# Performance work log

Measured on AMD Instinct MI355X. Metric: run time of the kernel, lower is better.

The kernel has to match this reference:

```python
import jax, jax.numpy as jnp
import numpy as np

B, S, E, H = 2, 2048, 1024, 16
D = E // H  # head_dim = 64
SCALE = D ** -0.5
NEG = -1e9


def setup_inputs() -> dict:
    key = jax.random.key(0)
    ks = jax.random.split(key, 10)
    hidden_states = jax.random.normal(ks[0], (B, S, E), dtype=jnp.float32)
    # CLIP-style additive causal mask [B, 1, L, S]
    causal = jnp.where(jnp.tril(jnp.ones((S, S), dtype=bool)), 0.0, NEG).astype(jnp.float32)
    attn_mask = jnp.broadcast_to(causal, (B, 1, S, S))
    def lin(kw, kb):
        W = jax.random.normal(kw, (E, E), dtype=jnp.float32) * (E ** -0.5)
        b = jax.random.normal(kb, (E,), dtype=jnp.float32) * 0.02
        return W, b
    Wq, bq = lin(ks[1], ks[2])
    Wk, bk = lin(ks[3], ks[4])
    Wv, bv = lin(ks[5], ks[6])
    Wo, bo = lin(ks[7], ks[8])
    return {"hidden_states": hidden_states, "attn_mask": attn_mask,
            "Wq": Wq, "bq": bq, "Wk": Wk, "bk": bk,
            "Wv": Wv, "bv": bv, "Wo": Wo, "bo": bo}


def reference(hidden_states, attn_mask, Wq, bq, Wk, bk, Wv, bv, Wo, bo):
    b, L, e = hidden_states.shape
    # projections (nn.Linear: x @ W.T + b)
    def split_heads(x):
        return x.reshape(b, L, H, D).transpose(0, 2, 1, 3)  # [b,h,l,d]
    q = split_heads(hidden_states @ Wq.T + bq)
    k = split_heads(hidden_states @ Wk.T + bk)
    v = split_heads(hidden_states @ Wv.T + bv)
    # QK^T * scale + additive mask, softmax, AV (dropout_p = 0 in eval)
    scores = jnp.einsum('bhld,bhsd->bhls', q, k) * SCALE + attn_mask
    attn = jax.nn.softmax(scores, axis=-1)
    ctx = jnp.einsum('bhls,bhsd->bhld', attn, v)
    ctx = ctx.transpose(0, 2, 1, 3).reshape(b, L, e)
    return ctx @ Wo.T + bo
```

## Files before the change

### kernel.cpp

```cpp
#include <hip/hip_runtime.h>
#include <hip/hip_bf16.h>
#include <stdint.h>


typedef __hip_bfloat16 bf16;
typedef short bf16x8 __attribute__((ext_vector_type(8)));
typedef short bf16x4 __attribute__((ext_vector_type(4)));
typedef float f32x4 __attribute__((ext_vector_type(4)));

__device__ __forceinline__ f32x4 mfma16(bf16x8 a, bf16x8 b, f32x4 c) {
  return __builtin_amdgcn_mfma_f32_16x16x32_bf16(a, b, c, 0, 0, 0);
}

__device__ __forceinline__ f32x4 mfma_k16(bf16x4 a, bf16x4 b, f32x4 c) {
#if __has_builtin(__builtin_amdgcn_mfma_f32_16x16x16bf16_1k)
  return __builtin_amdgcn_mfma_f32_16x16x16bf16_1k(a, b, c, 0, 0, 0);
#else
  f32x4 d;
  asm volatile("v_mfma_f32_16x16x16_bf16 %0, %1, %2, %3\n\ts_nop 7\n\ts_nop 7"
               : "=v"(d)
               : "v"(a), "v"(b), "v"(c));
  return d;
#endif
}

__device__ __forceinline__ void async16(const void* g, void* l) {
  __builtin_amdgcn_global_load_lds((const __attribute__((address_space(1))) void*)g,
                                   (__attribute__((address_space(3))) void*)l, 16, 0, 0);
}

__global__ __launch_bounds__(256) void cvt_kernel(
    const float* __restrict__ hs, const float* __restrict__ Wq,
    const float* __restrict__ Wk, const float* __restrict__ Wv,
    const float* __restrict__ Wo, bf16* __restrict__ dst) {
  const size_t e = ((size_t)blockIdx.x * 256 + threadIdx.x) * 8;
  const float* src;
  size_t off;
  if (e < 4194304) {
    src = hs; off = e;
  } else {
    const size_t w = e - 4194304;
    const int wi = (int)(w >> 20);
    src = (wi == 0) ? Wq : (wi == 1) ? Wk : (wi == 2) ? Wv : Wo;
    off = w & 1048575;
  }
  const float4 a = *(const float4*)(src + off);
  const float4 b = *(const float4*)(src + off + 4);
  union { bf16 h[8]; uint4 u; } p;
  p.h[0] = __float2bfloat16(a.x); p.h[1] = __float2bfloat16(a.y);
  p.h[2] = __float2bfloat16(a.z); p.h[3] = __float2bfloat16(a.w);
  p.h[4] = __float2bfloat16(b.x); p.h[5] = __float2bfloat16(b.y);
  p.h[6] = __float2bfloat16(b.z); p.h[7] = __float2bfloat16(b.w);
  *(uint4*)(dst + e) = p.u;
}

__global__ __launch_bounds__(256, 3) void qkv_gemm(
    const bf16* __restrict__ X, const bf16* __restrict__ Wb,
    const float* __restrict__ bq, const float* __restrict__ bk,
    const float* __restrict__ bv, bf16* __restrict__ out) {
  constexpr int Kd = 1024;
  __shared__ bf16 sA[2][128 * 32];
  __shared__ bf16 sB[2][128 * 32];
  const int tid = threadIdx.x;
  const int wave = tid >> 6, lane = tid & 63;
  const int g = lane >> 4, ln = lane & 15;
  const int tM = blockIdx.y * 128, tN = blockIdx.x * 128;
  const int which = tN >> 10;
  const bf16* W = Wb + (size_t)which * 1048576;
  const float* bias = (which == 0) ? bq : (which == 1) ? bk : bv;
  const int tNl = tN & 1023;
  const float oscale = (which == 0) ? 0.18033688011112042f : 1.0f;
  const int wrow = (wave >> 1) * 64, wcol = (wave & 1) * 64;
  const f32x4 fz = {0.f, 0.f, 0.f, 0.f};

  f32x4 acc[4][4];
#pragma unroll
  for (int i = 0; i < 4; ++i)
#pragma unroll
    for (int j = 0; j < 4; ++j) acc[i][j] = fz;

  int srow[4], scol[4];
#pragma unroll
  for (int t = 0; t < 4; ++t) {
    const int d = tid + t * 256;
    srow[t] = (d >> 2) & 127;
    scol[t] = ((d >> 9) << 5) + ((d & 3) << 3);
  }

  for (int k0 = 0; k0 < Kd; k0 += 64) {
    __syncthreads();
#pragma unroll
    for (int t = 0; t < 4; ++t) {
      const int d = tid + t * 256;
      async16(X + (size_t)(tM + srow[t]) * Kd + k0 + scol[t], &sA[0][0] + d * 8);
      async16(W + (size_t)(tNl + srow[t]) * Kd + k0 + scol[t], &sB[0][0] + d * 8);
    }
    __syncthreads();
#pragma unroll
    for (int kk = 0; kk < 2; ++kk) {
      bf16x8 aF[4], bF[4];
#pragma unroll
      for (int i = 0; i < 4; ++i)
        aF[i] = *(const bf16x8*)(&sA[kk][0] + (wrow + i * 16 + ln) * 32 + g * 8);
#pragma unroll
      for (int j = 0; j < 4; ++j)
        bF[j] = *(const bf16x8*)(&sB[kk][0] + (wcol + j * 16 + ln) * 32 + g * 8);
#pragma unroll
      for (int i = 0; i < 4; ++i)
#pragma unroll
        for (int j = 0; j < 4; ++j) acc[i][j] = mfma16(aF[i], bF[j], acc[i][j]);
    }
  }

  bf16* outw = out + (size_t)which * 4194304;
#pragma unroll
  for (int j = 0; j < 4; ++j) {
    const int nl = tNl + wcol + j * 16 + ln;
    const float bvf = bias[nl];
    const int h = nl >> 6, d = nl & 63;
#pragma unroll
    for (int i = 0; i < 4; ++i) {
#pragma unroll
      for (int r = 0; r < 4; ++r) {
        const int m = tM + wrow + i * 16 + g * 4 + r;
        const int b = m >> 11, s = m & 2047;
        const float v = (acc[i][j][r] + bvf) * oscale;
        outw[(((size_t)(b * 16 + h) * 2048 + s) << 6) + d] = __float2bfloat16(v);
      }
    }
  }
}

__global__ __launch_bounds__(256, 4) void out_gemm(
    const bf16* __restrict__ X, const bf16* __restrict__ W,
    const float* __restrict__ bias, float* __restrict__ out) {
  constexpr int Kd = 1024;
  __shared__ bf16 sA[64 * 32];
  __shared__ bf16 sB[64 * 32];
  const int tid = threadIdx.x;
  const int wave = tid >> 6, lane = tid & 63;
  const int g = lane >> 4, ln = lane & 15;
  const int tM = blockIdx.y * 64, tN = blockIdx.x * 64;
  const f32x4 fz = {0.f, 0.f, 0.f, 0.f};

  f32x4 acc[4];
#pragma unroll
  for (int j = 0; j < 4; ++j) acc[j] = fz;

  const int srow = tid >> 2, scol = (tid & 3) << 3;
  for (int k0 = 0; k0 < Kd; k0 += 32) {
    __syncthreads();
    async16(X + (size_t)(tM + srow) * Kd + k0 + scol, sA + tid * 8);
    async16(W + (size_t)(tN + srow) * Kd + k0 + scol, sB + tid * 8);
    __syncthreads();
    const bf16x8 aF = *(const bf16x8*)(sA + (wave * 16 + ln) * 32 + g * 8);
    bf16x8 bF[4];
#pragma unroll
    for (int j = 0; j < 4; ++j)
      bF[j] = *(const bf16x8*)(sB + (j * 16 + ln) * 32 + g * 8);
#pragma unroll
    for (int j = 0; j < 4; ++j) acc[j] = mfma16(aF, bF[j], acc[j]);
  }

#pragma unroll
  for (int j = 0; j < 4; ++j) {
    const int n = tN + j * 16 + ln;
    const float bvf = bias[n];
#pragma unroll
    for (int r = 0; r < 4; ++r) {
      const int m = tM + wave * 16 + g * 4 + r;
      out[(size_t)m * 1024 + n] = acc[j][r] + bvf;
    }
  }
}

__global__ __launch_bounds__(256, 4) void attn_kernel(
    const bf16* __restrict__ Q, const bf16* __restrict__ K,
    const bf16* __restrict__ V, bf16* __restrict__ O) {
  constexpr int S = 2048, D = 64;
  __shared__ bf16 sK[64 * 72];
  __shared__ bf16 sVf[64 * 64];

  const int tid = threadIdx.x;
  const int w = tid >> 6, lane = tid & 63;
  const int g = lane >> 4, ln = lane & 15;
  const int px = blockIdx.x, py = blockIdx.y;
  const int bh = (px & 7) * 4 + (py & 3);
  const int s = py >> 3;
  const int q0 = (px >> 3) + 4 * ((py >> 2) & 1);
  const int qt = (s == 0) ? 31 - q0
               : (s == 1) ? 16 + q0
               : (s == 2) ? 15 - q0
                          : q0;
  const int b = bh >> 4, h = bh & 15;
  const f32x4 fz = {0.f, 0.f, 0.f, 0.f};

  const bf16* Qb = Q + (size_t)bh * S * D;
  const bf16* Kb = K + (size_t)bh * S * D;
  const bf16* Vb = V + (size_t)bh * S * D;

  const int kr0 = tid >> 3, kc0 = (tid & 7) << 3;
  int vsrc[2][4], vdst[2];
#pragma unroll
  for (int t = 0; t < 2; ++t) {
    const int c = tid + t * 256;
    const int u = c * 2;
    const int kbdb = u >> 6, vg = (u >> 4) & 3, l0 = u & 15;
    const int kb = kbdb >> 2, db = kbdb & 3;
#pragma unroll
    for (int i = 0; i < 4; ++i) vsrc[t][i] = (kb * 16 + vg * 4 + i) * 64 + db * 16 + l0;
    vdst[t] = c * 8;
  }

  bf16x8 qf[2];
#pragma unroll
  for (int kc = 0; kc < 2; ++kc)
    qf[kc] = *(const bf16x8*)(Qb + (size_t)(qt * 64 + w * 16 + ln) * D + kc * 32 + g * 8);

  f32x4 oacc[4];
#pragma unroll
  for (int db = 0; db < 4; ++db) oacc[db] = fz;
  f32x4 lacc = fz;
  const short onebf = (short)0x3F80;
  const bf16x4 onesf = {onebf, onebf, onebf, onebf};

  uint4 kreg0 = *(const uint4*)(Kb + (size_t)kr0 * D + kc0);
  uint4 kreg1 = *(const uint4*)(Kb + (size_t)(kr0 + 32) * D + kc0);
  uint32_t vreg[2][4];
#pragma unroll
  for (int t = 0; t < 2; ++t)
#pragma unroll
    for (int i = 0; i < 4; ++i) vreg[t][i] = *(const uint32_t*)(Vb + vsrc[t][i]);

  for (int kt = 0; kt <= qt; ++kt) {
    __syncthreads();
    *(uint4*)(sK + kr0 * 72 + kc0) = kreg0;
    *(uint4*)(sK + (kr0 + 32) * 72 + kc0) = kreg1;
#pragma unroll
    for (int t = 0; t < 2; ++t) {
      const uint32_t d0 = vreg[t][0], d1 = vreg[t][1], d2 = vreg[t][2], d3 = vreg[t][3];
      uint4 pk;
      pk.x = (d1 << 16) | (d0 & 0xffffu);
      pk.y = (d3 << 16) | (d2 & 0xffffu);
      pk.z = (d1 & 0xffff0000u) | (d0 >> 16);
      pk.w = (d3 & 0xffff0000u) | (d2 >> 16);
      *(uint4*)(sVf + vdst[t]) = pk;
    }
    __syncthreads();
    if (kt < qt) {
      const size_t nb = (size_t)(kt + 1) * 64;
      kreg0 = *(const uint4*)(Kb + (nb + kr0) * D + kc0);
      kreg1 = *(const uint4*)(Kb + (nb + kr0 + 32) * D + kc0);
#pragma unroll
      for (int t = 0; t < 2; ++t)
#pragma unroll
        for (int i = 0; i < 4; ++i)
          vreg[t][i] = *(const uint32_t*)(Vb + nb * D + vsrc[t][i]);
    }

    f32x4 sacc[4];
#pragma unroll
    for (int kb = 0; kb < 4; ++kb) sacc[kb] = fz;
#pragma unroll
    for (int kb = 0; kb < 4; ++kb) {
      const bf16x8 k0 = *(const bf16x8*)(sK + (kb * 16 + ln) * 72 + g * 8);
      const bf16x8 k1 = *(const bf16x8*)(sK + (kb * 16 + ln) * 72 + 32 + g * 8);
      sacc[kb] = mfma16(k0, qf[0], sacc[kb]);
      sacc[kb] = mfma16(k1, qf[1], sacc[kb]);
    }

    const bool diag = (kt == qt);
    const int qloc = w * 16 + ln;
    bf16x4 pa[4];
#pragma unroll
    for (int kb = 0; kb < 4; ++kb) {
      union { bf16 hh[4]; bf16x4 v; } pu;
#pragma unroll
      for (int r = 0; r < 4; ++r) {
        float pv = exp2f(sacc[kb][r]);
        if (diag && (kb * 16 + g * 4 + r > qloc)) pv = 0.f;
        pu.hh[r] = __float2bfloat16(pv);
      }
      pa[kb] = pu.v;
      lacc = mfma_k16(pa[kb], onesf, lacc);
    }

#pragma unroll
    for (int db = 0; db < 4; ++db) {
#pragma unroll
      for (int kb = 0; kb < 4; ++kb) {
        const bf16x4 vf =
            *(const bf16x4*)(sVf + ((kb * 4 + db) * 64 + g * 16 + ln) * 4);
        oacc[db] = mfma_k16(pa[kb], vf, oacc[db]);
      }
    }
  }

  float invl[4];
#pragma unroll
  for (int r = 0; r < 4; ++r) invl[r] = 1.0f / lacc[r];

#pragma unroll
  for (int db = 0; db < 4; ++db)
#pragma unroll
    for (int r = 0; r < 4; ++r) {
      const int row = qt * 64 + w * 16 + g * 4 + r;
      const int col = db * 16 + ln;
      O[(((size_t)(b * 2048 + row) * 16 + h) << 6) + col] =
          __float2bfloat16(oacc[db][r] * invl[r]);
    }
}

extern "C" void kernel_launch(void* const* d_in, const int* in_sizes, int n_in,
                              void* d_out, int out_size, void* d_ws, size_t ws_size,
                              hipStream_t stream) {
  const float* hs = (const float*)d_in[0];
  const float* Wq = (const float*)d_in[2];
  const float* bq = (const float*)d_in[3];
  const float* Wk = (const float*)d_in[4];
  const float* bk = (const float*)d_in[5];
  const float* Wv = (const float*)d_in[6];
  const float* bv = (const float*)d_in[7];
  const float* Wo = (const float*)d_in[8];
  const float* bo = (const float*)d_in[9];
  float* out = (float*)d_out;

  char* ws = (char*)d_ws;
  bf16* XW = (bf16*)ws;
  bf16* Xb = XW;
  bf16* W3b = XW + 4194304;
  bf16* Wob = XW + 7340032;
  bf16* Qw = (bf16*)(ws + (16u << 20));
  bf16* Kw = (bf16*)(ws + (24u << 20));
  bf16* Vw = (bf16*)(ws + (32u << 20));
  bf16* Cw = (bf16*)ws;

  const dim3 blk(256);
  cvt_kernel<<<4096, blk, 0, stream>>>(hs, Wq, Wk, Wv, Wo, XW);
  qkv_gemm<<<dim3(24, 32), blk, 0, stream>>>(Xb, W3b, bq, bk, bv, Qw);
  attn_kernel<<<dim3(32, 32), blk, 0, stream>>>(Qw, Kw, Vw, Cw);
  out_gemm<<<dim3(16, 64), blk, 0, stream>>>(Cw, Wob, bo, out);
}
```

Baseline: 197.6 us.

## Store V pre-transposed and stream it into double-buffered swizzled LDS asynchronously

```diff
diff --git a/kernel.cpp b/kernel.cpp
--- a/kernel.cpp
+++ b/kernel.cpp
@@ -113,19 +113,37 @@
   }
 
   bf16* outw = out + (size_t)which * 4194304;
-#pragma unroll
-  for (int j = 0; j < 4; ++j) {
-    const int nl = tNl + wcol + j * 16 + ln;
-    const float bvf = bias[nl];
-    const int h = nl >> 6, d = nl & 63;
-#pragma unroll
-    for (int i = 0; i < 4; ++i) {
-#pragma unroll
-      for (int r = 0; r < 4; ++r) {
-        const int m = tM + wrow + i * 16 + g * 4 + r;
-        const int b = m >> 11, s = m & 2047;
-        const float v = (acc[i][j][r] + bvf) * oscale;
-        outw[(((size_t)(b * 16 + h) * 2048 + s) << 6) + d] = __float2bfloat16(v);
+  if (which == 2) {
+#pragma unroll
+    for (int j = 0; j < 4; ++j) {
+      const int nl = tNl + wcol + j * 16 + ln;
+      const float bvf = bias[nl];
+      const int h = nl >> 6, d = nl & 63;
+#pragma unroll
+      for (int i = 0; i < 4; ++i) {
+        const int m0 = tM + wrow + i * 16 + g * 4;
+        const int b = m0 >> 11, s0 = m0 & 2047;
+        union { bf16 hh[4]; bf16x4 v; } pk;
+#pragma unroll
+        for (int r = 0; r < 4; ++r) pk.hh[r] = __float2bfloat16(acc[i][j][r] + bvf);
+        *(bf16x4*)(outw + (((size_t)(b * 16 + h) * 64 + d) << 11) + s0) = pk.v;
+      }
+    }
+  } else {
+#pragma unroll
+    for (int j = 0; j < 4; ++j) {
+      const int nl = tNl + wcol + j * 16 + ln;
+      const float bvf = bias[nl];
+      const int h = nl >> 6, d = nl & 63;
+#pragma unroll
+      for (int i = 0; i < 4; ++i) {
+#pragma unroll
+        for (int r = 0; r < 4; ++r) {
+          const int m = tM + wrow + i * 16 + g * 4 + r;
+          const int b = m >> 11, s = m & 2047;
+          const float v = (acc[i][j][r] + bvf) * oscale;
+          outw[(((size_t)(b * 16 + h) * 2048 + s) << 6) + d] = __float2bfloat16(v);
+        }
       }
     }
   }
@@ -179,7 +197,7 @@
     const bf16* __restrict__ V, bf16* __restrict__ O) {
   constexpr int S = 2048, D = 64;
   __shared__ bf16 sK[64 * 72];
-  __shared__ bf16 sVf[64 * 64];
+  __shared__ bf16 sVt[2][64 * 64];
 
   const int tid = threadIdx.x;
   const int w = tid >> 6, lane = tid & 63;
@@ -197,19 +215,15 @@
 
   const bf16* Qb = Q + (size_t)bh * S * D;
   const bf16* Kb = K + (size_t)bh * S * D;
-  const bf16* Vb = V + (size_t)bh * S * D;
+  const bf16* Vt = V + (size_t)bh * 64 * 2048;
 
   const int kr0 = tid >> 3, kc0 = (tid & 7) << 3;
-  int vsrc[2][4], vdst[2];
+  int voff[2];
 #pragma unroll
   for (int t = 0; t < 2; ++t) {
-    const int c = tid + t * 256;
-    const int u = c * 2;
-    const int kbdb = u >> 6, vg = (u >> 4) & 3, l0 = u & 15;
-    const int kb = kbdb >> 2, db = kbdb & 3;
-#pragma unroll
-    for (int i = 0; i < 4; ++i) vsrc[t][i] = (kb * 16 + vg * 4 + i) * 64 + db * 16 + l0;
-    vdst[t] = c * 8;
+    const int p = tid + t * 256;
+    const int d = p >> 3, cc = p & 7;
+    voff[t] = d * 2048 + ((cc ^ ((d & 3) << 1)) << 3);
   }
 
   bf16x8 qf[2];
@@ -224,38 +238,31 @@
   const short onebf = (short)0x3F80;
   const bf16x4 onesf = {onebf, onebf, onebf, onebf};
 
+  int sx[4];
+  {
+    const int s8b = g >> 1, xr = (ln & 3) << 1, vlo = (g & 1) << 2;
+#pragma unroll
+    for (int kb = 0; kb < 4; ++kb) sx[kb] = (((2 * kb + s8b) ^ xr) << 3) + vlo;
+  }
+
   uint4 kreg0 = *(const uint4*)(Kb + (size_t)kr0 * D + kc0);
   uint4 kreg1 = *(const uint4*)(Kb + (size_t)(kr0 + 32) * D + kc0);
-  uint32_t vreg[2][4];
-#pragma unroll
-  for (int t = 0; t < 2; ++t)
-#pragma unroll
-    for (int i = 0; i < 4; ++i) vreg[t][i] = *(const uint32_t*)(Vb + vsrc[t][i]);
+  async16(Vt + voff[0], &sVt[0][0] + tid * 8);
+  async16(Vt + voff[1], &sVt[0][0] + (tid + 256) * 8);
 
   for (int kt = 0; kt <= qt; ++kt) {
     __syncthreads();
     *(uint4*)(sK + kr0 * 72 + kc0) = kreg0;
     *(uint4*)(sK + (kr0 + 32) * 72 + kc0) = kreg1;
-#pragma unroll
-    for (int t = 0; t < 2; ++t) {
-      const uint32_t d0 = vreg[t][0], d1 = vreg[t][1], d2 = vreg[t][2], d3 = vreg[t][3];
-      uint4 pk;
-      pk.x = (d1 << 16) | (d0 & 0xffffu);
-      pk.y = (d3 << 16) | (d2 & 0xffffu);
-      pk.z = (d1 & 0xffff0000u) | (d0 >> 16);
-      pk.w = (d3 & 0xffff0000u) | (d2 >> 16);
-      *(uint4*)(sVf + vdst[t]) = pk;
-    }
     __syncthreads();
     if (kt < qt) {
-      const size_t nb = (size_t)(kt + 1) * 64;
-      kreg0 = *(const uint4*)(Kb + (nb + kr0) * D + kc0);
-      kreg1 = *(const uint4*)(Kb + (nb + kr0 + 32) * D + kc0);
-#pragma unroll
-      for (int t = 0; t < 2; ++t)
-#pragma unroll
-        for (int i = 0; i < 4; ++i)
-          vreg[t][i] = *(const uint32_t*)(Vb + nb * D + vsrc[t][i]);
+      const int nb = (kt + 1) << 6;
+      bf16* vb = &sVt[(kt + 1) & 1][0];
+      async16(Vt + voff[0] + nb, vb + tid * 8);
+      async16(Vt + voff[1] + nb, vb + (tid + 256) * 8);
+      const size_t nr = (size_t)nb;
+      kreg0 = *(const uint4*)(Kb + (nr + kr0) * D + kc0);
+      kreg1 = *(const uint4*)(Kb + (nr + kr0 + 32) * D + kc0);
     }
 
     f32x4 sacc[4];
@@ -285,12 +292,13 @@
       lacc = mfma_k16(pa[kb], onesf, lacc);
     }
 
+    const bf16* sVc = &sVt[kt & 1][0];
 #pragma unroll
     for (int db = 0; db < 4; ++db) {
+      const int rowb = (db * 16 + ln) * 64;
 #pragma unroll
       for (int kb = 0; kb < 4; ++kb) {
-        const bf16x4 vf =
-            *(const bf16x4*)(sVf + ((kb * 4 + db) * 64 + g * 16 + ln) * 4);
+        const bf16x4 vf = *(const bf16x4*)(sVc + rowb + sx[kb]);
         oacc[db] = mfma_k16(pa[kb], vf, oacc[db]);
       }
     }
```

Measured after the change: 209.3 us. +5.9%, slower.

## Double-buffer shared memory tiles in QKV and output projection GEMMs

Applied to the files above, without the earlier changes.

```diff
diff --git a/kernel.cpp b/kernel.cpp
--- a/kernel.cpp
+++ b/kernel.cpp
@@ -79,37 +79,37 @@
 #pragma unroll
     for (int j = 0; j < 4; ++j) acc[i][j] = fz;
 
-  int srow[4], scol[4];
-#pragma unroll
-  for (int t = 0; t < 4; ++t) {
-    const int d = tid + t * 256;
-    srow[t] = (d >> 2) & 127;
-    scol[t] = ((d >> 9) << 5) + ((d & 3) << 3);
-  }
-
-  for (int k0 = 0; k0 < Kd; k0 += 64) {
+  const int r0 = tid >> 2, c0 = (tid & 3) << 3;
+
+  async16(X + (size_t)(tM + r0) * Kd + c0, &sA[0][0] + tid * 8);
+  async16(X + (size_t)(tM + r0 + 64) * Kd + c0, &sA[0][0] + (tid + 256) * 8);
+  async16(W + (size_t)(tNl + r0) * Kd + c0, &sB[0][0] + tid * 8);
+  async16(W + (size_t)(tNl + r0 + 64) * Kd + c0, &sB[0][0] + (tid + 256) * 8);
+  __syncthreads();
+
+  for (int k0 = 0; k0 < Kd; k0 += 32) {
+    const int cur = (k0 >> 5) & 1;
+    if (k0 + 32 < Kd) {
+      const int kn = k0 + 32;
+      bf16* an = &sA[cur ^ 1][0];
+      bf16* bn = &sB[cur ^ 1][0];
+      async16(X + (size_t)(tM + r0) * Kd + kn + c0, an + tid * 8);
+      async16(X + (size_t)(tM + r0 + 64) * Kd + kn + c0, an + (tid + 256) * 8);
+      async16(W + (size_t)(tNl + r0) * Kd + kn + c0, bn + tid * 8);
+      async16(W + (size_t)(tNl + r0 + 64) * Kd + kn + c0, bn + (tid + 256) * 8);
+    }
+    bf16x8 aF[4], bF[4];
+#pragma unroll
+    for (int i = 0; i < 4; ++i)
+      aF[i] = *(const bf16x8*)(&sA[cur][0] + (wrow + i * 16 + ln) * 32 + g * 8);
+#pragma unroll
+    for (int j = 0; j < 4; ++j)
+      bF[j] = *(const bf16x8*)(&sB[cur][0] + (wcol + j * 16 + ln) * 32 + g * 8);
+#pragma unroll
+    for (int i = 0; i < 4; ++i)
+#pragma unroll
+      for (int j = 0; j < 4; ++j) acc[i][j] = mfma16(aF[i], bF[j], acc[i][j]);
     __syncthreads();
-#pragma unroll
-    for (int t = 0; t < 4; ++t) {
-      const int d = tid + t * 256;
-      async16(X + (size_t)(tM + srow[t]) * Kd + k0 + scol[t], &sA[0][0] + d * 8);
-      async16(W + (size_t)(tNl + srow[t]) * Kd + k0 + scol[t], &sB[0][0] + d * 8);
-    }
-    __syncthreads();
-#pragma unroll
-    for (int kk = 0; kk < 2; ++kk) {
-      bf16x8 aF[4], bF[4];
-#pragma unroll
-      for (int i = 0; i < 4; ++i)
-        aF[i] = *(const bf16x8*)(&sA[kk][0] + (wrow + i * 16 + ln) * 32 + g * 8);
-#pragma unroll
-      for (int j = 0; j < 4; ++j)
-        bF[j] = *(const bf16x8*)(&sB[kk][0] + (wcol + j * 16 + ln) * 32 + g * 8);
-#pragma unroll
-      for (int i = 0; i < 4; ++i)
-#pragma unroll
-        for (int j = 0; j < 4; ++j) acc[i][j] = mfma16(aF[i], bF[j], acc[i][j]);
-    }
   }
 
   bf16* outw = out + (size_t)which * 4194304;
@@ -135,8 +135,8 @@
     const bf16* __restrict__ X, const bf16* __restrict__ W,
     const float* __restrict__ bias, float* __restrict__ out) {
   constexpr int Kd = 1024;
-  __shared__ bf16 sA[64 * 32];
-  __shared__ bf16 sB[64 * 32];
+  __shared__ bf16 sA[2][64 * 32];
+  __shared__ bf16 sB[2][64 * 32];
   const int tid = threadIdx.x;
   const int wave = tid >> 6, lane = tid & 63;
   const int g = lane >> 4, ln = lane & 15;
@@ -148,18 +148,24 @@
   for (int j = 0; j < 4; ++j) acc[j] = fz;
 
   const int srow = tid >> 2, scol = (tid & 3) << 3;
+  async16(X + (size_t)(tM + srow) * Kd + scol, &sA[0][0] + tid * 8);
+  async16(W + (size_t)(tN + srow) * Kd + scol, &sB[0][0] + tid * 8);
+  __syncthreads();
+
   for (int k0 = 0; k0 < Kd; k0 += 32) {
+    const int cur = (k0 >> 5) & 1;
+    if (k0 + 32 < Kd) {
+      async16(X + (size_t)(tM + srow) * Kd + k0 + 32 + scol, &sA[cur ^ 1][0] + tid * 8);
+      async16(W + (size_t)(tN + srow) * Kd + k0 + 32 + scol, &sB[cur ^ 1][0] + tid * 8);
+    }
+    const bf16x8 aF = *(const bf16x8*)(&sA[cur][0] + (wave * 16 + ln) * 32 + g * 8);
+    bf16x8 bF[4];
+#pragma unroll
+    for (int j = 0; j < 4; ++j)
+      bF[j] = *(const bf16x8*)(&sB[cur][0] + (j * 16 + ln) * 32 + g * 8);
+#pragma unroll
+    for (int j = 0; j < 4; ++j) acc[j] = mfma16(aF, bF[j], acc[j]);
     __syncthreads();
-    async16(X + (size_t)(tM + srow) * Kd + k0 + scol, sA + tid * 8);
-    async16(W + (size_t)(tN + srow) * Kd + k0 + scol, sB + tid * 8);
-    __syncthreads();
-    const bf16x8 aF = *(const bf16x8*)(sA + (wave * 16 + ln) * 32 + g * 8);
-    bf16x8 bF[4];
-#pragma unroll
-    for (int j = 0; j < 4; ++j)
-      bF[j] = *(const bf16x8*)(sB + (j * 16 + ln) * 32 + g * 8);
-#pragma unroll
-    for (int j = 0; j < 4; ++j) acc[j] = mfma16(aF, bF[j], acc[j]);
   }
 
 #pragma unroll
```

New measurement: 203.5 us. 3.0% more time.
